# Optimization experiments

Measured on AMD Instinct MI355X. Metric: run time of the kernel, lower is better.

The kernel has to match this reference:

```python
import jax, jax.numpy as jnp
import numpy as np

B, T, C, L = 512, 512, 96, 64
BLANK = C - 1          # keras ctc_batch_cost uses last class as blank
EPS = 1e-7             # keras.backend.epsilon()
NEG = -1e30            # log-space 'zero'


def setup_inputs() -> dict:
    key = jax.random.key(0)
    k1, k2, k3 = jax.random.split(key, 3)
    # y_pred is expected to be a softmax output (probabilities over classes)
    y_pred = jax.nn.softmax(jax.random.normal(k1, (B, T, C), dtype=jnp.float32), axis=-1)
    # labels exclude the blank class (values in [0, C-2])
    y_true = jax.random.randint(k2, (B, L), 0, C - 1).astype(jnp.int32)
    label_length = jax.random.randint(k3, (B, 1), 16, L + 1).astype(jnp.int32)
    # forward slices y_pred[:, 2:, :] -> effective time length T-2 = 510
    input_length = jnp.full((B, 1), T - 2, dtype=jnp.int32)
    return {"y_true": y_true, "y_pred": y_pred,
            "input_length": input_length, "label_length": label_length}


def _ctc_forward(logprobs, labels, input_len, label_len):
    """CTC negative log-likelihood via the forward (alpha) DP in log space.
    logprobs: [B, Tp, C] log-probabilities; labels: [B, L] int;
    input_len, label_len: [B] int. Returns [B] loss."""
    Bn, Tp, Cn = logprobs.shape
    Ln = labels.shape[1]
    S = 2 * Ln + 1
    s = jnp.arange(S)
    lab_idx = jnp.clip(s // 2, 0, Ln - 1)
    # extended label sequence: blank, l1, blank, l2, ..., blank  -> [B, S]
    ext = jnp.where(s[None, :] % 2 == 1, labels[:, lab_idx], BLANK)
    ext2 = jnp.concatenate([jnp.full((Bn, 2), -1, ext.dtype), ext[:, :-2]], axis=1)
    allow_skip = (ext != BLANK) & (ext != ext2)  # [B, S]

    # gather per-timestep log-probs of extended labels: [Tp, B, S]
    lp_t = jnp.transpose(logprobs, (1, 0, 2))
    lp_ext = jnp.take_along_axis(lp_t, jnp.broadcast_to(ext[None], (Tp, Bn, S)), axis=2)

    # t = 0 init: only s=0 (blank) and s=1 (first label) reachable
    alpha0 = jnp.where(s[None, :] < 2, lp_ext[0], NEG)  # [B, S]

    def step(alpha, xs):
        lp, t = xs
        a1 = jnp.concatenate([jnp.full((Bn, 1), NEG, alpha.dtype), alpha[:, :-1]], axis=1)
        a2 = jnp.concatenate([jnp.full((Bn, 2), NEG, alpha.dtype), alpha[:, :-2]], axis=1)
        a2 = jnp.where(allow_skip, a2, NEG)
        new = jnp.logaddexp(jnp.logaddexp(alpha, a1), a2) + lp
        # freeze alpha once past each sequence's input length
        alpha = jnp.where((t < input_len)[:, None], new, alpha)
        return alpha, None

    ts = jnp.arange(1, Tp)
    alpha, _ = jax.lax.scan(step, alpha0, (lp_ext[1:], ts))

    s_last = 2 * label_len  # index of final blank in extended sequence
    a_last = jnp.take_along_axis(alpha, s_last[:, None], axis=1)[:, 0]
    a_prev = jnp.take_along_axis(alpha, (s_last - 1)[:, None], axis=1)[:, 0]
    return -jnp.logaddexp(a_last, a_prev)


def reference(y_true, y_pred, input_length, label_length):
    # CTCLayer.call: crop first two timesteps, then keras ctc_batch_cost
    y_pred = y_pred[:, 2:, :]
    # keras: logits = log(probs + eps); tf.nn.ctc_loss then log-softmaxes internally
    logits = jnp.log(y_pred + EPS)
    logprobs = jax.nn.log_softmax(logits, axis=-1)
    loss = _ctc_forward(logprobs, y_true,
                        input_length.reshape(-1).astype(jnp.int32),
                        label_length.reshape(-1).astype(jnp.int32))
    return loss[:, None]  # [B, 1], matching ctc_batch_cost's expand_dims
```

## Files before the change

kernel.cpp:

```cpp
#include <hip/hip_runtime.h>


constexpr int   T_    = 512;
constexpr int   C_    = 96;
constexpr int   L_    = 64;
constexpr int   TP_   = 510;
constexpr float EPS_  = 1e-7f;
constexpr float LN2_  = 0.69314718055994530942f;
constexpr float LSE1_ = 1.3849806e-5f;

typedef float f8 __attribute__((ext_vector_type(8)));

__device__ __forceinline__ float flog2(float x) {
#if __has_builtin(__builtin_amdgcn_logf)
  return __builtin_amdgcn_logf(x);
#else
  return log2f(x);
#endif
}
__device__ __forceinline__ float fexp2(float x) {
#if __has_builtin(__builtin_amdgcn_exp2f)
  return __builtin_amdgcn_exp2f(x);
#else
  return exp2f(x);
#endif
}
__device__ __forceinline__ float fldexp(float x, int n) {
#if __has_builtin(__builtin_amdgcn_ldexpf)
  return __builtin_amdgcn_ldexpf(x, n);
#else
  return __builtin_ldexpf(x, n);
#endif
}

template<int CTRL, int RM, int BM, bool BC>
__device__ __forceinline__ float dppf(float old_, float src) {
  return __int_as_float(__builtin_amdgcn_update_dpp(
      __float_as_int(old_), __float_as_int(src), CTRL, RM, BM, BC));
}
template<int CTRL, int RM, int BM, bool BC>
__device__ __forceinline__ int dppi(int old_, int src) {
  return __builtin_amdgcn_update_dpp(old_, src, CTRL, RM, BM, BC);
}

__device__ __forceinline__ float lae2(float x, float y) {
  float m = fmaxf(x, y);
  return m + flog2(1.f + fexp2(-fabsf(x - y)));
}

#define LOADG(PL, PB, T0) {                                         \
  const float* _bl = colL + (size_t)(T0) * C_;                      \
  const float* _bb = colB + (size_t)(T0) * C_;                      \
  PL.s0 = _bl[0 * C_]; PB.s0 = _bb[0 * C_];                         \
  PL.s1 = _bl[1 * C_]; PB.s1 = _bb[1 * C_];                         \
  PL.s2 = _bl[2 * C_]; PB.s2 = _bb[2 * C_];                         \
  PL.s3 = _bl[3 * C_]; PB.s3 = _bb[3 * C_];                         \
  PL.s4 = _bl[4 * C_]; PB.s4 = _bb[4 * C_];                         \
  PL.s5 = _bl[5 * C_]; PB.s5 = _bb[5 * C_];                         \
  PL.s6 = _bl[6 * C_]; PB.s6 = _bb[6 * C_]; }                       \
  PL.s7 = *(colL + (size_t)((T0) + 7) * C_); PB.s7 = *(colB + (size_t)((T0) + 7) * C_);

#define LD1C(PL, PB, T0, J) {                                       \
  int _t = (T0) + (J); _t = _t < TP_ ? _t : TP_ - 1;                \
  PL.s##J = colL[(size_t)_t * C_]; PB.s##J = colB[(size_t)_t * C_]; }
#define LOADGC(PL, PB, T0) \
  LD1C(PL,PB,T0,0) LD1C(PL,PB,T0,1) LD1C(PL,PB,T0,2) LD1C(PL,PB,T0,3) \
  LD1C(PL,PB,T0,4) LD1C(PL,PB,T0,5) LD1C(PL,PB,T0,6) LD1C(PL,PB,T0,7)

#define A8(PL, PB) { stepF(PL.s0,PB.s0); stepF(PL.s1,PB.s1);        \
  stepF(PL.s2,PB.s2); stepF(PL.s3,PB.s3); stepF(PL.s4,PB.s4);       \
  stepF(PL.s5,PB.s5); stepF(PL.s6,PB.s6); stepF(PL.s7,PB.s7); }

#define B8(PL, PB) { stepS(PL.s0,PB.s0); stepS(PL.s1,PB.s1);        \
  stepS(PL.s2,PB.s2); stepS(PL.s3,PB.s3); renormS();                \
  stepS(PL.s4,PB.s4); stepS(PL.s5,PB.s5); stepS(PL.s6,PB.s6);       \
  stepS(PL.s7,PB.s7); renormS(); }

#define TAIL1(PL, PB, J, OFF) \
  if ((tb + (OFF) + (J)) < tmax) stepF(PL.s##J, PB.s##J);
#define TAIL8(PL, PB, OFF) \
  TAIL1(PL,PB,0,OFF) TAIL1(PL,PB,1,OFF) TAIL1(PL,PB,2,OFF) TAIL1(PL,PB,3,OFF) \
  TAIL1(PL,PB,4,OFF) TAIL1(PL,PB,5,OFF) TAIL1(PL,PB,6,OFF) TAIL1(PL,PB,7,OFF)

__global__ __launch_bounds__(64, 1) void ctc_fwd(
    const int* __restrict__ y_true, const float* __restrict__ y_pred,
    const int* __restrict__ input_len, const int* __restrict__ label_len,
    float* __restrict__ out)
{
  const int b = blockIdx.x;
  const int l = threadIdx.x;

  const float* __restrict__ rp = y_pred + (size_t)b * T_ * C_ + 2 * C_;
  const int  lab     = y_true[b * L_ + l];
  const int  labPrev = __shfl_up(lab, 1);
  const bool skipOK  = (l >= 1) && (lab != labPrev);
  const int  ilen    = input_len[b];
  const int  llen    = label_len[b];
  const int  tmax    = ilen < TP_ ? ilen : TP_;

  const float* __restrict__ colL = rp + lab;
  const float* __restrict__ colB = rp + (C_ - 1);

  float mE, mO, mX = 0.f;
  int   e = 0, d = 0;

  mE = (l == 0) ? (colB[0] + EPS_) : 0.f;
  mO = (l == 0) ? (colL[0] + EPS_) : 0.f;

  f8 pl0, pl1, pl2, pl3, pb0, pb1, pb2, pb3;
  LOADG(pl0, pb0, 1);  LOADG(pl1, pb1, 9);
  LOADG(pl2, pb2, 17); LOADG(pl3, pb3, 25);

  auto runDP = [&](auto has128) {
    constexpr bool H128 = decltype(has128)::value;

    auto stepF = [&](float pl, float pb) {
      float plE = pl + EPS_, pbE = pb + EPS_;
      int   e1  = dppi<0x138, 0xf, 0xf, false>(0, e);
      float m1  = dppf<0x138, 0xf, 0xf, false>(0.f, mO);
      int   dd  = e1 - e;  dd = dd < 120 ? dd : 120;
      float a1  = fldexp(m1, dd);
      float a1s = skipOK ? a1 : 0.f;
      float nE  = (mE + a1) * pbE;
      float nO  = ((mO + mE) + a1s) * plE;
      float nX = 0.f, mx;
      if constexpr (H128) { nX = (mX + mO) * pbE; mx = fmaxf(fmaxf(nE, nO), nX); }
      else                { mx = fmaxf(nE, nO); }
      int  kb = __float_as_int(mx) >> 23;
      int  ks = 127 - kb;
      bool z  = (mx == 0.f);
      e  = z ? e1 : (e + kb - 127);
      mE = fldexp(nE, ks);
      mO = fldexp(nO, ks);
      if constexpr (H128) mX = fldexp(nX, ks);
    };

    auto stepS = [&](float pl, float pb) {
      float plE = pl + EPS_, pbE = pb + EPS_;
      float m1  = dppf<0x138, 0xf, 0xf, false>(0.f, mO);
      float a1  = fldexp(m1, d);
      float a1s = skipOK ? a1 : 0.f;
      float nE  = (mE + a1) * pbE;
      float nO  = ((mO + mE) + a1s) * plE;
      if constexpr (H128) mX = (mX + mO) * pbE;
      mE = nE; mO = nO;
    };

    auto renormS = [&]() {
      float mx = fmaxf(mE, mO);
      if constexpr (H128) mx = fmaxf(mx, mX);
      int kb = __float_as_int(mx) >> 23;
      int ks = 127 - kb;
      e += kb - 127;
      mE = fldexp(mE, ks);
      mO = fldexp(mO, ks);
      if constexpr (H128) mX = fldexp(mX, ks);
      int e1 = dppi<0x138, 0xf, 0xf, false>(0, e);
      int dd = e1 - e;  d = dd < 120 ? dd : 120;
    };

    int tb = 1;
#pragma unroll 1
    for (; tb < 65 && tb + 64 <= tmax; tb += 32) {
      A8(pl0, pb0); LOADG(pl0, pb0, tb + 32);
      A8(pl1, pb1); LOADG(pl1, pb1, tb + 40);
      A8(pl2, pb2); LOADG(pl2, pb2, tb + 48);
      A8(pl3, pb3); LOADG(pl3, pb3, tb + 56);
    }
    renormS();
#pragma unroll 1
    for (; tb + 64 <= tmax; tb += 32) {
      B8(pl0, pb0); LOADG(pl0, pb0, tb + 32);
      B8(pl1, pb1); LOADG(pl1, pb1, tb + 40);
      B8(pl2, pb2); LOADG(pl2, pb2, tb + 48);
      B8(pl3, pb3); LOADG(pl3, pb3, tb + 56);
    }
#pragma unroll 1
    for (; tb + 32 <= tmax; tb += 32) {
      A8(pl0, pb0); LOADGC(pl0, pb0, tb + 32);
      A8(pl1, pb1); LOADGC(pl1, pb1, tb + 40);
      A8(pl2, pb2); LOADGC(pl2, pb2, tb + 48);
      A8(pl3, pb3); LOADGC(pl3, pb3, tb + 56);
    }
    TAIL8(pl0, pb0, 0); TAIL8(pl1, pb1, 8);
    TAIL8(pl2, pb2, 16); TAIL8(pl3, pb3, 24);
  };

  if (llen >= 64) runDP(std::integral_constant<bool, true>{});
  else            runDP(std::integral_constant<bool, false>{});

  float ef  = (float)e;
  float lgE = flog2(mE) + ef;
  float lgO = flog2(mO) + ef;
  float aL;
  if (llen >= 64) { float lgX = flog2(mX) + ef; aL = __shfl(lgX, 63); }
  else            { aL = __shfl(lgE, llen); }
  float aP = __shfl(lgO, llen - 1);
  if (l == 0)
    out[b] = -LN2_ * (lae2(aL, aP) - (float)tmax * LSE1_);
}

extern "C" void kernel_launch(void* const* d_in, const int* in_sizes, int n_in,
                              void* d_out, int out_size, void* d_ws, size_t ws_size,
                              hipStream_t stream) {
  const int*   y_true = (const int*)d_in[0];
  const float* y_pred = (const float*)d_in[1];
  const int*   ilen   = (const int*)d_in[2];
  const int*   llen   = (const int*)d_in[3];
  float*       outp   = (float*)d_out;
  const int    B      = out_size;
  hipLaunchKernelGGL(ctc_fwd, dim3(B), dim3(64), 0, stream,
                     y_true, y_pred, ilen, llen, outp);
}
```

Before: 35.06 us.

## Interleave two batch items per wavefront to hide the serial DP latency

Each 64-lane block now runs the CTC alpha recurrence for two batch items at once, interleaving their independent dependency chains so one chain's DPP, ldexp and multiply latency overlaps with the other's. The grid is halved to B/2 blocks. The skip select becomes an fma with a 0/1 mask, and the slow renorm now guards against an all-zero max. The cost is double the register use for prefetch buffers, fewer waves (256 on a chip with many CUs), and the H128 path running for both items whenever either has full label length.

```diff
diff --git a/kernel.cpp b/kernel.cpp
--- a/kernel.cpp
+++ b/kernel.cpp
@@ -48,156 +48,171 @@
   return m + flog2(1.f + fexp2(-fabsf(x - y)));
 }
 
-#define LOADG(PL, PB, T0) {                                         \
-  const float* _bl = colL + (size_t)(T0) * C_;                      \
-  const float* _bb = colB + (size_t)(T0) * C_;                      \
-  PL.s0 = _bl[0 * C_]; PB.s0 = _bb[0 * C_];                         \
-  PL.s1 = _bl[1 * C_]; PB.s1 = _bb[1 * C_];                         \
-  PL.s2 = _bl[2 * C_]; PB.s2 = _bb[2 * C_];                         \
-  PL.s3 = _bl[3 * C_]; PB.s3 = _bb[3 * C_];                         \
-  PL.s4 = _bl[4 * C_]; PB.s4 = _bb[4 * C_];                         \
-  PL.s5 = _bl[5 * C_]; PB.s5 = _bb[5 * C_];                         \
-  PL.s6 = _bl[6 * C_]; PB.s6 = _bb[6 * C_]; }                       \
-  PL.s7 = *(colL + (size_t)((T0) + 7) * C_); PB.s7 = *(colB + (size_t)((T0) + 7) * C_);
-
-#define LD1C(PL, PB, T0, J) {                                       \
-  int _t = (T0) + (J); _t = _t < TP_ ? _t : TP_ - 1;                \
-  PL.s##J = colL[(size_t)_t * C_]; PB.s##J = colB[(size_t)_t * C_]; }
-#define LOADGC(PL, PB, T0) \
-  LD1C(PL,PB,T0,0) LD1C(PL,PB,T0,1) LD1C(PL,PB,T0,2) LD1C(PL,PB,T0,3) \
-  LD1C(PL,PB,T0,4) LD1C(PL,PB,T0,5) LD1C(PL,PB,T0,6) LD1C(PL,PB,T0,7)
-
-#define A8(PL, PB) { stepF(PL.s0,PB.s0); stepF(PL.s1,PB.s1);        \
-  stepF(PL.s2,PB.s2); stepF(PL.s3,PB.s3); stepF(PL.s4,PB.s4);       \
-  stepF(PL.s5,PB.s5); stepF(PL.s6,PB.s6); stepF(PL.s7,PB.s7); }
-
-#define B8(PL, PB) { stepS(PL.s0,PB.s0); stepS(PL.s1,PB.s1);        \
-  stepS(PL.s2,PB.s2); stepS(PL.s3,PB.s3); renormS();                \
-  stepS(PL.s4,PB.s4); stepS(PL.s5,PB.s5); stepS(PL.s6,PB.s6);       \
-  stepS(PL.s7,PB.s7); renormS(); }
-
-#define TAIL1(PL, PB, J, OFF) \
-  if ((tb + (OFF) + (J)) < tmax) stepF(PL.s##J, PB.s##J);
-#define TAIL8(PL, PB, OFF) \
-  TAIL1(PL,PB,0,OFF) TAIL1(PL,PB,1,OFF) TAIL1(PL,PB,2,OFF) TAIL1(PL,PB,3,OFF) \
-  TAIL1(PL,PB,4,OFF) TAIL1(PL,PB,5,OFF) TAIL1(PL,PB,6,OFF) TAIL1(PL,PB,7,OFF)
-
-__global__ __launch_bounds__(64, 1) void ctc_fwd(
+#define LOADG(PL, PB, CL, CB, T0) {                                  \
+  const float* _bl = (CL) + (size_t)(T0) * C_;                       \
+  const float* _bb = (CB) + (size_t)(T0) * C_;                       \
+  PL.s0=_bl[0*C_]; PB.s0=_bb[0*C_]; PL.s1=_bl[1*C_]; PB.s1=_bb[1*C_];\
+  PL.s2=_bl[2*C_]; PB.s2=_bb[2*C_]; PL.s3=_bl[3*C_]; PB.s3=_bb[3*C_];\
+  PL.s4=_bl[4*C_]; PB.s4=_bb[4*C_]; PL.s5=_bl[5*C_]; PB.s5=_bb[5*C_];\
+  PL.s6=_bl[6*C_]; PB.s6=_bb[6*C_]; PL.s7=_bl[7*C_]; PB.s7=_bb[7*C_]; }
+
+#define LD1C(PL, PB, CL, CB, T0, J) {                                \
+  int _t = (T0) + (J); _t = _t < TP_ ? _t : TP_ - 1;                 \
+  PL.s##J = (CL)[(size_t)_t * C_]; PB.s##J = (CB)[(size_t)_t * C_]; }
+#define LOADGC(PL, PB, CL, CB, T0)                                   \
+  LD1C(PL,PB,CL,CB,T0,0) LD1C(PL,PB,CL,CB,T0,1) LD1C(PL,PB,CL,CB,T0,2) \
+  LD1C(PL,PB,CL,CB,T0,3) LD1C(PL,PB,CL,CB,T0,4) LD1C(PL,PB,CL,CB,T0,5) \
+  LD1C(PL,PB,CL,CB,T0,6) LD1C(PL,PB,CL,CB,T0,7)
+
+#define LOADJ(G, T0)  LOADG(pl##G##A, pb##G##A, colLA, colBA, T0) \
+                      LOADG(pl##G##B, pb##G##B, colLB, colBB, T0)
+#define LOADJC(G, T0) LOADGC(pl##G##A, pb##G##A, colLA, colBA, T0) \
+                      LOADGC(pl##G##B, pb##G##B, colLB, colBB, T0)
+
+#define JF(G, J) \
+  stepF(pl##G##A.s##J, pb##G##A.s##J, mEA, mOA, mXA, eA, skipMA); \
+  stepF(pl##G##B.s##J, pb##G##B.s##J, mEB, mOB, mXB, eB, skipMB);
+#define A8J(G) { JF(G,0) JF(G,1) JF(G,2) JF(G,3) JF(G,4) JF(G,5) JF(G,6) JF(G,7) }
+
+#define RNS() { renormS(mEA, mOA, mXA, eA, dA); renormS(mEB, mOB, mXB, eB, dB); }
+#define JS(G, J) \
+  stepS(pl##G##A.s##J, pb##G##A.s##J, mEA, mOA, mXA, dA, skipMA); \
+  stepS(pl##G##B.s##J, pb##G##B.s##J, mEB, mOB, mXB, dB, skipMB);
+#define B8J(G) { JS(G,0) JS(G,1) JS(G,2) JS(G,3) RNS() JS(G,4) JS(G,5) JS(G,6) JS(G,7) RNS() }
+
+#define TJ(G, J, OFF) \
+  if ((tb + (OFF) + (J)) < tmaxA) stepF(pl##G##A.s##J, pb##G##A.s##J, mEA, mOA, mXA, eA, skipMA); \
+  if ((tb + (OFF) + (J)) < tmaxB) stepF(pl##G##B.s##J, pb##G##B.s##J, mEB, mOB, mXB, eB, skipMB);
+#define T8J(G, OFF) { TJ(G,0,OFF) TJ(G,1,OFF) TJ(G,2,OFF) TJ(G,3,OFF) \
+                      TJ(G,4,OFF) TJ(G,5,OFF) TJ(G,6,OFF) TJ(G,7,OFF) }
+
+#define PDECL(P, BEXPR) \
+  const int  b##P = (BEXPR); \
+  const float* __restrict__ rp##P = y_pred + (size_t)b##P * T_ * C_ + 2 * C_; \
+  const int  lab##P = y_true[b##P * L_ + l]; \
+  const int  labPrev##P = __shfl_up(lab##P, 1); \
+  const float skipM##P = (l >= 1 && lab##P != labPrev##P) ? 1.f : 0.f; \
+  const int  ilen##P = input_len[b##P]; \
+  const int  llen##P = label_len[b##P]; \
+  const int  tmax##P = ilen##P < TP_ ? ilen##P : TP_; \
+  const float* __restrict__ colL##P = rp##P + lab##P; \
+  const float* __restrict__ colB##P = rp##P + (C_ - 1); \
+  float mE##P, mO##P, mX##P = 0.f; int e##P = 0, d##P = 0; \
+  mE##P = (l == 0) ? (colB##P[0] + EPS_) : 0.f; \
+  mO##P = (l == 0) ? (colL##P[0] + EPS_) : 0.f;
+
+#define READOUT(P) { \
+  float ef  = (float)e##P; \
+  float lgE = flog2(mE##P) + ef; \
+  float lgO = flog2(mO##P) + ef; \
+  float aL; \
+  if (llen##P >= 64) { float lgX = flog2(mX##P) + ef; aL = __shfl(lgX, 63); } \
+  else               { aL = __shfl(lgE, llen##P); } \
+  float aP = __shfl(lgO, llen##P - 1); \
+  if (l == 0) out[b##P] = -LN2_ * (lae2(aL, aP) - (float)tmax##P * LSE1_); }
+
+__global__ __launch_bounds__(64, 1) void ctc_fwd2(
     const int* __restrict__ y_true, const float* __restrict__ y_pred,
     const int* __restrict__ input_len, const int* __restrict__ label_len,
     float* __restrict__ out)
 {
-  const int b = blockIdx.x;
   const int l = threadIdx.x;
 
-  const float* __restrict__ rp = y_pred + (size_t)b * T_ * C_ + 2 * C_;
-  const int  lab     = y_true[b * L_ + l];
-  const int  labPrev = __shfl_up(lab, 1);
-  const bool skipOK  = (l >= 1) && (lab != labPrev);
-  const int  ilen    = input_len[b];
-  const int  llen    = label_len[b];
-  const int  tmax    = ilen < TP_ ? ilen : TP_;
-
-  const float* __restrict__ colL = rp + lab;
-  const float* __restrict__ colB = rp + (C_ - 1);
-
-  float mE, mO, mX = 0.f;
-  int   e = 0, d = 0;
-
-  mE = (l == 0) ? (colB[0] + EPS_) : 0.f;
-  mO = (l == 0) ? (colL[0] + EPS_) : 0.f;
-
-  f8 pl0, pl1, pl2, pl3, pb0, pb1, pb2, pb3;
-  LOADG(pl0, pb0, 1);  LOADG(pl1, pb1, 9);
-  LOADG(pl2, pb2, 17); LOADG(pl3, pb3, 25);
-
-  auto runDP = [&](auto has128) {
-    constexpr bool H128 = decltype(has128)::value;
-
-    auto stepF = [&](float pl, float pb) {
+  PDECL(A, blockIdx.x)
+  PDECL(B, blockIdx.x + gridDim.x)
+
+  f8 pl0A, pl1A, pl2A, pl3A, pb0A, pb1A, pb2A, pb3A;
+  f8 pl0B, pl1B, pl2B, pl3B, pb0B, pb1B, pb2B, pb3B;
+  LOADJ(0, 1)  LOADJ(1, 9)  LOADJ(2, 17)  LOADJ(3, 25)
+
+  const int tmn = tmaxA < tmaxB ? tmaxA : tmaxB;
+
+  auto runDP = [&](auto hasC) {
+    constexpr bool H128 = decltype(hasC)::value;
+
+    auto stepF = [&](float pl, float pb, float& mE, float& mO, float& mX,
+                     int& e, float skipM) {
       float plE = pl + EPS_, pbE = pb + EPS_;
-      int   e1  = dppi<0x138, 0xf, 0xf, false>(0, e);
+      int   en  = dppi<0x138, 0xf, 0xf, false>(0, e);
       float m1  = dppf<0x138, 0xf, 0xf, false>(0.f, mO);
-      int   dd  = e1 - e;  dd = dd < 120 ? dd : 120;
+      int   dd  = en - e;  dd = dd < 120 ? dd : 120;
       float a1  = fldexp(m1, dd);
-      float a1s = skipOK ? a1 : 0.f;
       float nE  = (mE + a1) * pbE;
-      float nO  = ((mO + mE) + a1s) * plE;
+      float nO  = fmaf(a1, skipM, mO + mE) * plE;
       float nX = 0.f, mx;
       if constexpr (H128) { nX = (mX + mO) * pbE; mx = fmaxf(fmaxf(nE, nO), nX); }
       else                { mx = fmaxf(nE, nO); }
       int  kb = __float_as_int(mx) >> 23;
       int  ks = 127 - kb;
       bool z  = (mx == 0.f);
-      e  = z ? e1 : (e + kb - 127);
+      e  = z ? en : (e + kb - 127);
       mE = fldexp(nE, ks);
       mO = fldexp(nO, ks);
       if constexpr (H128) mX = fldexp(nX, ks);
     };
 
-    auto stepS = [&](float pl, float pb) {
+    auto stepS = [&](float pl, float pb, float& mE, float& mO, float& mX,
+                     int d, float skipM) {
       float plE = pl + EPS_, pbE = pb + EPS_;
       float m1  = dppf<0x138, 0xf, 0xf, false>(0.f, mO);
       float a1  = fldexp(m1, d);
-      float a1s = skipOK ? a1 : 0.f;
       float nE  = (mE + a1) * pbE;
-      float nO  = ((mO + mE) + a1s) * plE;
+      float nO  = fmaf(a1, skipM, mO + mE) * plE;
       if constexpr (H128) mX = (mX + mO) * pbE;
       mE = nE; mO = nO;
     };
 
-    auto renormS = [&]() {
+    auto renormS = [&](float& mE, float& mO, float& mX, int& e, int& d) {
       float mx = fmaxf(mE, mO);
       if constexpr (H128) mx = fmaxf(mx, mX);
-      int kb = __float_as_int(mx) >> 23;
-      int ks = 127 - kb;
-      e += kb - 127;
+      int  kb = __float_as_int(mx) >> 23;
+      bool z  = (mx == 0.f);
+      int  ks = z ? 0 : (127 - kb);
+      e = z ? e : (e + kb - 127);
       mE = fldexp(mE, ks);
       mO = fldexp(mO, ks);
       if constexpr (H128) mX = fldexp(mX, ks);
-      int e1 = dppi<0x138, 0xf, 0xf, false>(0, e);
-      int dd = e1 - e;  d = dd < 120 ? dd : 120;
+      int en = dppi<0x138, 0xf, 0xf, false>(0, e);
+      int dd = en - e;  d = dd < 120 ? dd : 120;
     };
 
     int tb = 1;
 #pragma unroll 1
-    for (; tb < 65 && tb + 64 <= tmax; tb += 32) {
-      A8(pl0, pb0); LOADG(pl0, pb0, tb + 32);
-      A8(pl1, pb1); LOADG(pl1, pb1, tb + 40);
-      A8(pl2, pb2); LOADG(pl2, pb2, tb + 48);
-      A8(pl3, pb3); LOADG(pl3, pb3, tb + 56);
+    for (; tb < 65 && tb + 64 <= tmn; tb += 32) {
+      A8J(0) LOADJ(0, tb + 32)
+      A8J(1) LOADJ(1, tb + 40)
+      A8J(2) LOADJ(2, tb + 48)
+      A8J(3) LOADJ(3, tb + 56)
     }
-    renormS();
-#pragma unroll 1
-    for (; tb + 64 <= tmax; tb += 32) {
-      B8(pl0, pb0); LOADG(pl0, pb0, tb + 32);
-      B8(pl1, pb1); LOADG(pl1, pb1, tb + 40);
-      B8(pl2, pb2); LOADG(pl2, pb2, tb + 48);
-      B8(pl3, pb3); LOADG(pl3, pb3, tb + 56);
+    RNS()
+#pragma unroll 1
+    for (; tb + 64 <= tmn; tb += 32) {
+      B8J(0) LOADJ(0, tb + 32)
+      B8J(1) LOADJ(1, tb + 40)
+      B8J(2) LOADJ(2, tb + 48)
+      B8J(3) LOADJ(3, tb + 56)
     }
 #pragma unroll 1
-    for (; tb + 32 <= tmax; tb += 32) {
-      A8(pl0, pb0); LOADGC(pl0, pb0, tb + 32);
-      A8(pl1, pb1); LOADGC(pl1, pb1, tb + 40);
-      A8(pl2, pb2); LOADGC(pl2, pb2, tb + 48);
-      A8(pl3, pb3); LOADGC(pl3, pb3, tb + 56);
+    for (; tb + 32 <= tmn; tb += 32) {
+      A8J(0) LOADJC(0, tb + 32)
+      A8J(1) LOADJC(1, tb + 40)
+      A8J(2) LOADJC(2, tb + 48)
+      A8J(3) LOADJC(3, tb + 56)
     }
-    TAIL8(pl0, pb0, 0); TAIL8(pl1, pb1, 8);
-    TAIL8(pl2, pb2, 16); TAIL8(pl3, pb3, 24);
+    T8J(0, 0) T8J(1, 8) T8J(2, 16) T8J(3, 24)
+#pragma unroll 1
+    for (int t = tb + 32; t < tmaxA; ++t)
+      stepF(colLA[(size_t)t * C_], colBA[(size_t)t * C_], mEA, mOA, mXA, eA, skipMA);
+#pragma unroll 1
+    for (int t = tb + 32; t < tmaxB; ++t)
+      stepF(colLB[(size_t)t * C_], colBB[(size_t)t * C_], mEB, mOB, mXB, eB, skipMB);
   };
 
-  if (llen >= 64) runDP(std::integral_constant<bool, true>{});
-  else            runDP(std::integral_constant<bool, false>{});
-
-  float ef  = (float)e;
-  float lgE = flog2(mE) + ef;
-  float lgO = flog2(mO) + ef;
-  float aL;
-  if (llen >= 64) { float lgX = flog2(mX) + ef; aL = __shfl(lgX, 63); }
-  else            { aL = __shfl(lgE, llen); }
-  float aP = __shfl(lgO, llen - 1);
-  if (l == 0)
-    out[b] = -LN2_ * (lae2(aL, aP) - (float)tmax * LSE1_);
+  if (llenA >= 64 || llenB >= 64) runDP(std::integral_constant<bool, true>{});
+  else                            runDP(std::integral_constant<bool, false>{});
+
+  READOUT(A)
+  READOUT(B)
 }
 
 extern "C" void kernel_launch(void* const* d_in, const int* in_sizes, int n_in,
@@ -209,6 +224,6 @@
   const int*   llen   = (const int*)d_in[3];
   float*       outp   = (float*)d_out;
   const int    B      = out_size;
-  hipLaunchKernelGGL(ctc_fwd, dim3(B), dim3(64), 0, stream,
+  hipLaunchKernelGGL(ctc_fwd2, dim3(B / 2), dim3(64), 0, stream,
                      y_true, y_pred, ilen, llen, outp);
 }
```

After: 101.5 us. 190% more time.

## Stage per-timestep rows into LDS ring via async global_load_lds

Applied to the files above, without the earlier changes.

Replaces the per-lane strided global gathers of label and blank probabilities with 24 lanes copying whole 96-float timestep rows into a 6-slot LDS ring using the global_load_lds builtin, with manual vmcnt waits. Each lane then reads its column from LDS. The 32-step loop structure is replaced by 8-step groups with a uniform steady/guarded compute path. It also swaps the skip select for an fma with a 0/1 mask and makes renormalization zero-safe. It trades coalesced wide loads for LDS reads and hand-tuned waitcnt, with the risk of synchronization mistakes.

```diff
diff --git a/kernel.cpp b/kernel.cpp
--- a/kernel.cpp
+++ b/kernel.cpp
@@ -48,88 +48,104 @@
   return m + flog2(1.f + fexp2(-fabsf(x - y)));
 }
 
-#define LOADG(PL, PB, T0) {                                         \
-  const float* _bl = colL + (size_t)(T0) * C_;                      \
-  const float* _bb = colB + (size_t)(T0) * C_;                      \
-  PL.s0 = _bl[0 * C_]; PB.s0 = _bb[0 * C_];                         \
-  PL.s1 = _bl[1 * C_]; PB.s1 = _bb[1 * C_];                         \
-  PL.s2 = _bl[2 * C_]; PB.s2 = _bb[2 * C_];                         \
-  PL.s3 = _bl[3 * C_]; PB.s3 = _bb[3 * C_];                         \
-  PL.s4 = _bl[4 * C_]; PB.s4 = _bb[4 * C_];                         \
-  PL.s5 = _bl[5 * C_]; PB.s5 = _bb[5 * C_];                         \
-  PL.s6 = _bl[6 * C_]; PB.s6 = _bb[6 * C_]; }                       \
-  PL.s7 = *(colL + (size_t)((T0) + 7) * C_); PB.s7 = *(colB + (size_t)((T0) + 7) * C_);
-
-#define LD1C(PL, PB, T0, J) {                                       \
-  int _t = (T0) + (J); _t = _t < TP_ ? _t : TP_ - 1;                \
-  PL.s##J = colL[(size_t)_t * C_]; PB.s##J = colB[(size_t)_t * C_]; }
-#define LOADGC(PL, PB, T0) \
-  LD1C(PL,PB,T0,0) LD1C(PL,PB,T0,1) LD1C(PL,PB,T0,2) LD1C(PL,PB,T0,3) \
-  LD1C(PL,PB,T0,4) LD1C(PL,PB,T0,5) LD1C(PL,PB,T0,6) LD1C(PL,PB,T0,7)
-
-#define A8(PL, PB) { stepF(PL.s0,PB.s0); stepF(PL.s1,PB.s1);        \
-  stepF(PL.s2,PB.s2); stepF(PL.s3,PB.s3); stepF(PL.s4,PB.s4);       \
-  stepF(PL.s5,PB.s5); stepF(PL.s6,PB.s6); stepF(PL.s7,PB.s7); }
-
-#define B8(PL, PB) { stepS(PL.s0,PB.s0); stepS(PL.s1,PB.s1);        \
-  stepS(PL.s2,PB.s2); stepS(PL.s3,PB.s3); renormS();                \
-  stepS(PL.s4,PB.s4); stepS(PL.s5,PB.s5); stepS(PL.s6,PB.s6);       \
-  stepS(PL.s7,PB.s7); renormS(); }
-
-#define TAIL1(PL, PB, J, OFF) \
-  if ((tb + (OFF) + (J)) < tmax) stepF(PL.s##J, PB.s##J);
-#define TAIL8(PL, PB, OFF) \
-  TAIL1(PL,PB,0,OFF) TAIL1(PL,PB,1,OFF) TAIL1(PL,PB,2,OFF) TAIL1(PL,PB,3,OFF) \
-  TAIL1(PL,PB,4,OFF) TAIL1(PL,PB,5,OFF) TAIL1(PL,PB,6,OFF) TAIL1(PL,PB,7,OFF)
+__device__ __forceinline__ void gload_lds16(const float* g, float* lds_) {
+  __builtin_amdgcn_global_load_lds(
+      (const __attribute__((address_space(1))) void*)g,
+      (__attribute__((address_space(3))) void*)lds_,
+      16, 0, 0);
+}
+
+#define WAITV(N) asm volatile("s_waitcnt vmcnt(" #N ")" ::: "memory")
+
+#define DSRING(SLOT, PL, PB) {                                   \
+  const float* _pl = smem + (SLOT) * 768 + lab;                  \
+  const float* _pb = smem + (SLOT) * 768 + 95;                   \
+  PL.s0 = _pl[0];   PB.s0 = _pb[0];                              \
+  PL.s1 = _pl[96];  PB.s1 = _pb[96];                             \
+  PL.s2 = _pl[192]; PB.s2 = _pb[192];                            \
+  PL.s3 = _pl[288]; PB.s3 = _pb[288];                            \
+  PL.s4 = _pl[384]; PB.s4 = _pb[384];                            \
+  PL.s5 = _pl[480]; PB.s5 = _pb[480];                            \
+  PL.s6 = _pl[576]; PB.s6 = _pb[576];                            \
+  PL.s7 = _pl[672]; PB.s7 = _pb[672]; }
+
+#define STEADY8(PL, PB) { renormS();                             \
+  stepS(PL.s0,PB.s0); stepS(PL.s1,PB.s1);                        \
+  stepS(PL.s2,PB.s2); stepS(PL.s3,PB.s3); renormS();             \
+  stepS(PL.s4,PB.s4); stepS(PL.s5,PB.s5);                        \
+  stepS(PL.s6,PB.s6); stepS(PL.s7,PB.s7); }
+
+#define GUARD8(T0, PL, PB) {                                     \
+  if ((T0)+0 < tmax) stepF(PL.s0,PB.s0);                         \
+  if ((T0)+1 < tmax) stepF(PL.s1,PB.s1);                         \
+  if ((T0)+2 < tmax) stepF(PL.s2,PB.s2);                         \
+  if ((T0)+3 < tmax) stepF(PL.s3,PB.s3);                         \
+  if ((T0)+4 < tmax) stepF(PL.s4,PB.s4);                         \
+  if ((T0)+5 < tmax) stepF(PL.s5,PB.s5);                         \
+  if ((T0)+6 < tmax) stepF(PL.s6,PB.s6);                         \
+  if ((T0)+7 < tmax) stepF(PL.s7,PB.s7); }
+
+#define COMPUTEG(K, PL, PB) { const int _t0 = 1 + 8*(K);         \
+  if ((K) >= 8 && (_t0 + 7) < tmax) { STEADY8(PL, PB) }          \
+  else                              { GUARD8(_t0, PL, PB) } }
 
 __global__ __launch_bounds__(64, 1) void ctc_fwd(
     const int* __restrict__ y_true, const float* __restrict__ y_pred,
     const int* __restrict__ input_len, const int* __restrict__ label_len,
     float* __restrict__ out)
 {
+  __shared__ float smem[6 * 768];
   const int b = blockIdx.x;
   const int l = threadIdx.x;
 
   const float* __restrict__ rp = y_pred + (size_t)b * T_ * C_ + 2 * C_;
   const int  lab     = y_true[b * L_ + l];
   const int  labPrev = __shfl_up(lab, 1);
-  const bool skipOK  = (l >= 1) && (lab != labPrev);
+  const float skipM  = (l >= 1 && lab != labPrev) ? 1.f : 0.f;
   const int  ilen    = input_len[b];
   const int  llen    = label_len[b];
   const int  tmax    = ilen < TP_ ? ilen : TP_;
 
-  const float* __restrict__ colL = rp + lab;
-  const float* __restrict__ colB = rp + (C_ - 1);
+  auto stage = [&](int g, int slot) {
+    const int t0 = 1 + g * 8;
+    float* dst = smem + slot * 768;
+    if (l < 24) {
+      const float* s0 = rp + 4 * l;
+      int t;
+      t = t0 + 0; t = t < TP_ ? t : TP_ - 1; gload_lds16(s0 + (size_t)t * C_, dst + 0 * 96);
+      t = t0 + 1; t = t < TP_ ? t : TP_ - 1; gload_lds16(s0 + (size_t)t * C_, dst + 1 * 96);
+      t = t0 + 2; t = t < TP_ ? t : TP_ - 1; gload_lds16(s0 + (size_t)t * C_, dst + 2 * 96);
+      t = t0 + 3; t = t < TP_ ? t : TP_ - 1; gload_lds16(s0 + (size_t)t * C_, dst + 3 * 96);
+      t = t0 + 4; t = t < TP_ ? t : TP_ - 1; gload_lds16(s0 + (size_t)t * C_, dst + 4 * 96);
+      t = t0 + 5; t = t < TP_ ? t : TP_ - 1; gload_lds16(s0 + (size_t)t * C_, dst + 5 * 96);
+      t = t0 + 6; t = t < TP_ ? t : TP_ - 1; gload_lds16(s0 + (size_t)t * C_, dst + 6 * 96);
+      t = t0 + 7; t = t < TP_ ? t : TP_ - 1; gload_lds16(s0 + (size_t)t * C_, dst + 7 * 96);
+    }
+  };
 
   float mE, mO, mX = 0.f;
   int   e = 0, d = 0;
-
-  mE = (l == 0) ? (colB[0] + EPS_) : 0.f;
-  mO = (l == 0) ? (colL[0] + EPS_) : 0.f;
-
-  f8 pl0, pl1, pl2, pl3, pb0, pb1, pb2, pb3;
-  LOADG(pl0, pb0, 1);  LOADG(pl1, pb1, 9);
-  LOADG(pl2, pb2, 17); LOADG(pl3, pb3, 25);
-
-  auto runDP = [&](auto has128) {
-    constexpr bool H128 = decltype(has128)::value;
+  mE = (l == 0) ? (rp[C_ - 1] + EPS_) : 0.f;
+  mO = (l == 0) ? (rp[lab] + EPS_) : 0.f;
+
+  auto runDP = [&](auto hasC) {
+    constexpr bool H128 = decltype(hasC)::value;
 
     auto stepF = [&](float pl, float pb) {
       float plE = pl + EPS_, pbE = pb + EPS_;
-      int   e1  = dppi<0x138, 0xf, 0xf, false>(0, e);
+      int   en  = dppi<0x138, 0xf, 0xf, false>(0, e);
       float m1  = dppf<0x138, 0xf, 0xf, false>(0.f, mO);
-      int   dd  = e1 - e;  dd = dd < 120 ? dd : 120;
+      int   dd  = en - e;  dd = dd < 120 ? dd : 120;
       float a1  = fldexp(m1, dd);
-      float a1s = skipOK ? a1 : 0.f;
       float nE  = (mE + a1) * pbE;
-      float nO  = ((mO + mE) + a1s) * plE;
+      float nO  = fmaf(a1, skipM, mO + mE) * plE;
       float nX = 0.f, mx;
       if constexpr (H128) { nX = (mX + mO) * pbE; mx = fmaxf(fmaxf(nE, nO), nX); }
       else                { mx = fmaxf(nE, nO); }
       int  kb = __float_as_int(mx) >> 23;
       int  ks = 127 - kb;
       bool z  = (mx == 0.f);
-      e  = z ? e1 : (e + kb - 127);
+      e  = z ? en : (e + kb - 127);
       mE = fldexp(nE, ks);
       mO = fldexp(nO, ks);
       if constexpr (H128) mX = fldexp(nX, ks);
@@ -139,9 +155,8 @@
       float plE = pl + EPS_, pbE = pb + EPS_;
       float m1  = dppf<0x138, 0xf, 0xf, false>(0.f, mO);
       float a1  = fldexp(m1, d);
-      float a1s = skipOK ? a1 : 0.f;
       float nE  = (mE + a1) * pbE;
-      float nO  = ((mO + mE) + a1s) * plE;
+      float nO  = fmaf(a1, skipM, mO + mE) * plE;
       if constexpr (H128) mX = (mX + mO) * pbE;
       mE = nE; mO = nO;
     };
@@ -149,41 +164,35 @@
     auto renormS = [&]() {
       float mx = fmaxf(mE, mO);
       if constexpr (H128) mx = fmaxf(mx, mX);
-      int kb = __float_as_int(mx) >> 23;
-      int ks = 127 - kb;
-      e += kb - 127;
+      int  kb = __float_as_int(mx) >> 23;
+      bool z  = (mx == 0.f);
+      int  ks = z ? 0 : (127 - kb);
+      e = z ? e : (e + kb - 127);
       mE = fldexp(mE, ks);
       mO = fldexp(mO, ks);
       if constexpr (H128) mX = fldexp(mX, ks);
-      int e1 = dppi<0x138, 0xf, 0xf, false>(0, e);
-      int dd = e1 - e;  d = dd < 120 ? dd : 120;
+      int en = dppi<0x138, 0xf, 0xf, false>(0, e);
+      int dd = en - e;  d = dd < 120 ? dd : 120;
     };
 
-    int tb = 1;
+    stage(0, 0); stage(1, 1); stage(2, 2); stage(3, 3); stage(4, 4);
+    WAITV(32);
+    f8 plA, pbA, plB, pbB;
+    DSRING(0, plA, pbA);
+
+    int sR = 1, sS = 5, gS = 5;
 #pragma unroll 1
-    for (; tb < 65 && tb + 64 <= tmax; tb += 32) {
-      A8(pl0, pb0); LOADG(pl0, pb0, tb + 32);
-      A8(pl1, pb1); LOADG(pl1, pb1, tb + 40);
-      A8(pl2, pb2); LOADG(pl2, pb2, tb + 48);
-      A8(pl3, pb3); LOADG(pl3, pb3, tb + 56);
+    for (int k = 0; k < 64; k += 2) {
+      WAITV(24);
+      DSRING(sR, plB, pbB); sR = (sR == 5) ? 0 : sR + 1;
+      COMPUTEG(k, plA, pbA);
+      stage(gS <= 63 ? gS : 63, sS); sS = (sS == 5) ? 0 : sS + 1; ++gS;
+
+      WAITV(24);
+      DSRING(sR, plA, pbA); sR = (sR == 5) ? 0 : sR + 1;
+      COMPUTEG(k + 1, plB, pbB);
+      stage(gS <= 63 ? gS : 63, sS); sS = (sS == 5) ? 0 : sS + 1; ++gS;
     }
-    renormS();
-#pragma unroll 1
-    for (; tb + 64 <= tmax; tb += 32) {
-      B8(pl0, pb0); LOADG(pl0, pb0, tb + 32);
-      B8(pl1, pb1); LOADG(pl1, pb1, tb + 40);
-      B8(pl2, pb2); LOADG(pl2, pb2, tb + 48);
-      B8(pl3, pb3); LOADG(pl3, pb3, tb + 56);
-    }
-#pragma unroll 1
-    for (; tb + 32 <= tmax; tb += 32) {
-      A8(pl0, pb0); LOADGC(pl0, pb0, tb + 32);
-      A8(pl1, pb1); LOADGC(pl1, pb1, tb + 40);
-      A8(pl2, pb2); LOADGC(pl2, pb2, tb + 48);
-      A8(pl3, pb3); LOADGC(pl3, pb3, tb + 56);
-    }
-    TAIL8(pl0, pb0, 0); TAIL8(pl1, pb1, 8);
-    TAIL8(pl2, pb2, 16); TAIL8(pl3, pb3, 24);
   };
 
   if (llen >= 64) runDP(std::integral_constant<bool, true>{});
```

Result: slower. 39.77 us (+13.4%).
